# Performance work log

Hardware: AMD Instinct MI355X
Metric: run time of the kernel (lower is better)

The kernel has to match this reference:

```python
import jax, jax.numpy as jnp
import numpy as np
import math

B, CK, T, H, W = 4, 64, 8, 30, 54
N, CV = 8, 512

def setup_inputs() -> dict:
    key = jax.random.key(0)
    k1, k2, k3, k4 = jax.random.split(key, 4)
    mem_keys = jax.random.normal(k1, (B, CK, T, H, W), dtype=jnp.float32)
    mem_values = jax.random.normal(k2, (N, CV, T, H, W), dtype=jnp.float32)
    qk = jax.random.normal(k3, (B, CK, H, W), dtype=jnp.float32)
    broadcast_map = jax.random.randint(k4, (N,), 0, B, dtype=jnp.int64)
    return {"mem_keys": mem_keys, "mem_values": mem_values, "qk": qk,
            "broadcast_map": broadcast_map}

def reference(mem_keys, mem_values, qk, broadcast_map):
    # STCNModel.read_memory
    Bq, CKq, Tq, Hq, Wq = mem_keys.shape
    mk = mem_keys.reshape(Bq, CKq, Tq * Hq * Wq)      # [B, CK, THW]
    q = qk.reshape(Bq, CKq, Hq * Wq)                   # [B, CK, HW]
    a_sq = jnp.sum(mk * mk, axis=1)[:, :, None]        # [B, THW, 1]
    ab = jnp.einsum('bct,bcq->btq', mk, q)             # [B, THW, HW]
    frame_affinity = (2.0 * ab - a_sq) / math.sqrt(CKq)
    # softmax over memory dim (axis=1)
    frame_affinity = jax.nn.softmax(frame_affinity, axis=1)
    obj_affinity = frame_affinity[broadcast_map]       # [N, THW, HW]
    Nn, CVv = mem_values.shape[0], mem_values.shape[1]
    mo = mem_values.reshape(Nn, CVv, Tq * Hq * Wq)     # [N, CV, THW]
    obj_read = jnp.einsum('nct,ntq->ncq', mo, obj_affinity)
    return obj_read.reshape(Nn, CVv, Hq, Wq)
```

## Files before the change

kernel.cpp:

```cpp
#include <hip/hip_runtime.h>
#include <hip/hip_bf16.h>

#define CKDIM 64
#define THW   12960
#define HWDIM 1620
#define NOBJ  8
#define CVAL  512
#define NB    4
#define NSTEP 405
#define NJT   13
#define NCHS  8
#define NCHP  4
#define PCH   16
#define S2F   0.3606737602222409f

using bf16x8 = __attribute__((ext_vector_type(8))) short;
using f32x4  = __attribute__((ext_vector_type(4))) float;

__device__ __forceinline__ unsigned cvtpk(float lo, float hi) {
    unsigned r;
    asm("v_cvt_pk_bf16_f32 %0, %1, %2" : "=v"(r) : "v"(lo), "v"(hi));
    return r;
}
__device__ __forceinline__ unsigned short bf_rne(float x) {
    unsigned u = __float_as_uint(x);
    u += 0x7FFFu + ((u >> 16) & 1u);
    return (unsigned short)(u >> 16);
}
__device__ __forceinline__ float fexp2(float x) {
#if __has_builtin(__builtin_amdgcn_exp2f)
    return __builtin_amdgcn_exp2f(x);
#else
    return __expf(x * 0.69314718055994531f);
#endif
}

__global__ void stcn_ksq_kernel(const float* __restrict__ mk, float* __restrict__ k8l) {
    int t = blockIdx.x * 256 + threadIdx.x;
    if (t >= THW) return;
    int b = blockIdx.y;
    const float* p = mk + (size_t)b * CKDIM * THW + t;
    float s = 0.f;
#pragma unroll
    for (int c = 0; c < CKDIM; ++c) { float v = p[(size_t)c * THW]; s = fmaf(v, v, s); }
    k8l[b * THW + t] = s * (0.125f * 1.44269504088896341f);
}

__global__ __launch_bounds__(512)
void stcn_ktr_kernel(const float* __restrict__ mk, unsigned short* __restrict__ kbt) {
    __shared__ unsigned short L[64][72];
    const int tid = threadIdx.x, b = blockIdx.y, t0 = blockIdx.x * 64;
#pragma unroll
    for (int it = 0; it < 8; ++it) {
        int idx = tid + 512 * it;
        int tt = idx & 63, c = idx >> 6;
        int t = t0 + tt;
        float v = (t < THW) ? mk[((size_t)b * CKDIM + c) * THW + t] : 0.f;
        L[tt][c] = bf_rne(v);
    }
    __syncthreads();
    int tt = tid >> 3, cq = tid & 7;
    int t = t0 + tt;
    if (t < THW) {
        uint4 o = *(const uint4*)&L[tt][8 * cq];
        *(uint4*)(kbt + ((size_t)b * THW + t) * CKDIM + 8 * cq) = o;
    }
}

__global__ void stcn_vcvt_kernel(const float* __restrict__ mv, unsigned short* __restrict__ mvb) {
    size_t i = ((size_t)blockIdx.x * 256 + threadIdx.x) * 8;
    if (i >= (size_t)NOBJ * CVAL * THW) return;
    float4 v0 = *(const float4*)(mv + i);
    float4 v1 = *(const float4*)(mv + i + 4);
    uint4 o;
    o.x = cvtpk(v0.x, v0.y); o.y = cvtpk(v0.z, v0.w);
    o.z = cvtpk(v1.x, v1.y); o.w = cvtpk(v1.z, v1.w);
    *(uint4*)(mvb + i) = o;
}

template <int MODE, bool VB16, bool KB16>
__global__ __launch_bounds__(512, (MODE == 1) ? 4 : 1)
void stcn_aff_kernel(const float* __restrict__ mk, const unsigned short* __restrict__ kbt,
                     const float* __restrict__ qk, const float* __restrict__ k8l,
                     float* __restrict__ mpart, float* __restrict__ lpart,
                     const float* __restrict__ mv, const unsigned short* __restrict__ mvb,
                     const int* __restrict__ bmap, float* __restrict__ out)
{
    constexpr int SMEM_BYTES = (MODE == 0) ? 36864 : 45312;
    __shared__ __align__(16) unsigned char smem[SMEM_BYTES];
    unsigned short* KtP   = (unsigned short*)smem;
    float*          k8tP  = (float*)(smem + 9216);
    unsigned short* PtP   = (unsigned short*)(smem + 9472);
    unsigned short* VtP   = (unsigned short*)(smem + 23808);
    float*          mjsP  = (float*)(smem + 44288);
    float*          iljsP = (float*)(smem + 44800);
    unsigned short* QtP   = (unsigned short*)smem;

    const int tid  = threadIdx.x;
    const int w    = tid >> 6;
    const int lane = tid & 63;
    const int g    = lane >> 4;
    const int lr   = lane & 15;

    int b, n = 0, jt, kc, cb = 0;
    if (MODE == 0) { b = blockIdx.y; jt = blockIdx.x >> 3; kc = blockIdx.x & 7; }
    else {
        n = blockIdx.y; jt = blockIdx.x >> 3; kc = (blockIdx.x >> 1) & 3; cb = blockIdx.x & 1;
        b = bmap[n];
    }
    const int jbase = jt * 128;
    const int cbase = cb * 256;

#pragma unroll
    for (int it = 0; it < 8; ++it) {
        int idx = tid + 512 * it;
        int j = idx & 127, cp = idx >> 7;
        int jg = jbase + j;
        float q0 = 0.f, q1 = 0.f;
        if (jg < HWDIM) {
            const float* qp = qk + ((size_t)b * CKDIM + 2 * cp) * HWDIM + jg;
            q0 = qp[0]; q1 = qp[HWDIM];
        }
        unsigned wh = cvtpk(q0, q1);
        float r0 = q0 - __uint_as_float(wh << 16);
        float r1 = q1 - __uint_as_float(wh & 0xFFFF0000u);
        *(unsigned*)&QtP[(0 * 128 + j) * 72 + 2 * cp] = wh;
        *(unsigned*)&QtP[(1 * 128 + j) * 72 + 2 * cp] = cvtpk(r0, r1);
    }
    __syncthreads();
    bf16x8 bqh[2], bql[2];
#pragma unroll
    for (int s = 0; s < 2; ++s) {
        bqh[s] = *(const bf16x8*)&QtP[(0 * 128 + w * 16 + lr) * 72 + 32 * s + 8 * g];
        bql[s] = *(const bf16x8*)&QtP[(1 * 128 + w * 16 + lr) * 72 + 32 * s + 8 * g];
    }
    __syncthreads();

    auto stageK_loads = [&](int st, uint2& k16, float2* kvf) {
        if constexpr (KB16) {
            int tt = tid >> 4, cq = tid & 15;
            k16 = *(const uint2*)(kbt + ((size_t)b * THW + st * 32 + tt) * CKDIM + 4 * cq);
        } else {
#pragma unroll
            for (int it = 0; it < 2; ++it) {
                int idx = tid + 512 * it;
                int tt = idx & 31, cp = idx >> 5;
                const float* kp = mk + ((size_t)b * CKDIM + 2 * cp) * THW + st * 32 + tt;
                kvf[it].x = kp[0];
                kvf[it].y = kp[THW];
            }
        }
    };
    auto stageK_write = [&](int buf, uint2 k16, const float2* kvf) {
        if constexpr (KB16) {
            int tt = tid >> 4, cq = tid & 15;
            *(uint2*)&KtP[(buf * 32 + tt) * 72 + 4 * cq] = k16;
        } else {
#pragma unroll
            for (int it = 0; it < 2; ++it) {
                int idx = tid + 512 * it;
                int tt = idx & 31, cp = idx >> 5;
                *(unsigned*)&KtP[(buf * 32 + tt) * 72 + 2 * cp] = cvtpk(kvf[it].x, kvf[it].y);
            }
        }
    };

    int s0, s1;
    if (MODE == 0) { s0 = (NSTEP * kc) / NCHS; s1 = (NSTEP * (kc + 1)) / NCHS; }
    else           { s0 = (NSTEP * kc) / NCHP; s1 = (NSTEP * (kc + 1)) / NCHP; }

    if (MODE == 1 && tid < 128) {
        int jg = jbase + tid;
        float m = 0.f, l = 0.f;
        if (jg < HWDIM) {
            m = -1e30f;
#pragma unroll
            for (int c = 0; c < NCHS; ++c) {
                float mc = mpart[(b * NCHS + c) * HWDIM + jg];
                float lc = lpart[(b * NCHS + c) * HWDIM + jg];
                float mn = fmaxf(m, mc);
                l = l * fexp2(m - mn) + lc * fexp2(mc - mn);
                m = mn;
            }
        }
        mjsP[tid]  = m;
        iljsP[tid] = (l > 0.f) ? 1.f / l : 0.f;
    }
    {
        uint2 k16; float2 kvf[2];
        stageK_loads(s0, k16, kvf);
        stageK_write(0, k16, kvf);
        if (tid < 32) k8tP[tid] = k8l[b * THW + s0 * 32 + tid];
    }
    __syncthreads();

    float mv_j = 0.f, il_j = 0.f;
    if (MODE == 1) { mv_j = mjsP[w * 16 + lr]; il_j = iljsP[w * 16 + lr]; }

    float m_run = -1e30f, l_run = 0.f;
    f32x4 zz = {0.f, 0.f, 0.f, 0.f};
    f32x4 acc[4][4];
    if (MODE == 1)
#pragma unroll
        for (int i = 0; i < 4; ++i)
#pragma unroll
            for (int j = 0; j < 4; ++j) acc[i][j] = zz;

    const int wc = w >> 1, wj = w & 1;
    const int vc = tid >> 1, vth = tid & 1;

    int cur = 0;
    for (int st = s0; st < s1; ++st) {
        const int t0 = st * 32;
        const bool nxt = (st + 1 < s1);

        uint4 vw0 = {0,0,0,0}, vw1 = {0,0,0,0};
        if (MODE == 1) {
            if (VB16) {
                const unsigned short* vp = mvb + ((size_t)n * CVAL + cbase + vc) * THW + t0 + vth * 16;
                vw0 = *(const uint4*)vp;
                vw1 = *(const uint4*)(vp + 8);
            } else {
                const float* vp = mv + ((size_t)n * CVAL + cbase + vc) * THW + t0 + vth * 16;
                float4 f0 = *(const float4*)vp;
                float4 f1 = *(const float4*)(vp + 4);
                float4 f2 = *(const float4*)(vp + 8);
                float4 f3 = *(const float4*)(vp + 12);
                vw0 = make_uint4(cvtpk(f0.x,f0.y), cvtpk(f0.z,f0.w), cvtpk(f1.x,f1.y), cvtpk(f1.z,f1.w));
                vw1 = make_uint4(cvtpk(f2.x,f2.y), cvtpk(f2.z,f2.w), cvtpk(f3.x,f3.y), cvtpk(f3.z,f3.w));
            }
        }
        uint2 k16; float2 kvf[2];
        float k8next = 0.f;
        if (nxt) {
            stageK_loads(st + 1, k16, kvf);
            if (tid < 32) k8next = k8l[b * THW + (st + 1) * 32 + tid];
        }
        bf16x8 ak0[2], ak1[2];
#pragma unroll
        for (int s = 0; s < 2; ++s) {
            ak0[s] = *(const bf16x8*)&KtP[(cur * 32 + lr) * 72 + 32 * s + 8 * g];
            ak1[s] = *(const bf16x8*)&KtP[(cur * 32 + 16 + lr) * 72 + 32 * s + 8 * g];
        }
        f32x4 k80 = *(const f32x4*)&k8tP[cur * 32 + 4 * g];
        f32x4 k81 = *(const f32x4*)&k8tP[cur * 32 + 16 + 4 * g];
        f32x4 ab0 = zz, ab1 = zz;
#pragma unroll
        for (int s = 0; s < 2; ++s) {
            ab0 = __builtin_amdgcn_mfma_f32_16x16x32_bf16(ak0[s], bqh[s], ab0, 0, 0, 0);
            ab0 = __builtin_amdgcn_mfma_f32_16x16x32_bf16(ak0[s], bql[s], ab0, 0, 0, 0);
            ab1 = __builtin_amdgcn_mfma_f32_16x16x32_bf16(ak1[s], bqh[s], ab1, 0, 0, 0);
            ab1 = __builtin_amdgcn_mfma_f32_16x16x32_bf16(ak1[s], bql[s], ab1, 0, 0, 0);
        }
        if (nxt) {
            stageK_write(cur ^ 1, k16, kvf);
            if (tid < 32) k8tP[(cur ^ 1) * 32 + tid] = k8next;
        }

        if (MODE == 0) {
            float L0[4], L1[4], tmax = -1e30f;
#pragma unroll
            for (int r = 0; r < 4; ++r) {
                L0[r] = fmaf(ab0[r], S2F, -k80[r]); tmax = fmaxf(tmax, L0[r]);
                L1[r] = fmaf(ab1[r], S2F, -k81[r]); tmax = fmaxf(tmax, L1[r]);
            }
            float ps = 0.f;
#pragma unroll
            for (int r = 0; r < 4; ++r)
                ps += fexp2(L0[r] - tmax) + fexp2(L1[r] - tmax);
            float mn = fmaxf(m_run, tmax);
            l_run = l_run * fexp2(m_run - mn) + ps * fexp2(tmax - mn);
            m_run = mn;
            __syncthreads();
        } else {
            float p0[4], p1[4];
#pragma unroll
            for (int r = 0; r < 4; ++r) {
                p0[r] = fexp2(fmaf(ab0[r], S2F, -k80[r]) - mv_j) * il_j;
                p1[r] = fexp2(fmaf(ab1[r], S2F, -k81[r]) - mv_j) * il_j;
            }
            __syncthreads();
            {
                int jl = w * 16 + lr;
                *(uint2*)&PtP[jl * 56 + 4 * g]      = make_uint2(cvtpk(p0[0], p0[1]), cvtpk(p0[2], p0[3]));
                *(uint2*)&PtP[jl * 56 + 16 + 4 * g] = make_uint2(cvtpk(p1[0], p1[1]), cvtpk(p1[2], p1[3]));
                *(uint4*)&VtP[vc * 40 + vth * 16]     = vw0;
                *(uint4*)&VtP[vc * 40 + vth * 16 + 8] = vw1;
            }
            __syncthreads();
            bf16x8 bp[4];
#pragma unroll
            for (int jf = 0; jf < 4; ++jf)
                bp[jf] = *(const bf16x8*)&PtP[(wj * 64 + jf * 16 + lr) * 56 + 8 * g];
#pragma unroll
            for (int cf = 0; cf < 4; ++cf) {
                bf16x8 av = *(const bf16x8*)&VtP[(wc * 64 + cf * 16 + lr) * 40 + 8 * g];
#pragma unroll
                for (int jf = 0; jf < 4; ++jf)
                    acc[cf][jf] = __builtin_amdgcn_mfma_f32_16x16x32_bf16(av, bp[jf], acc[cf][jf], 0, 0, 0);
            }
        }
        cur ^= 1;
    }

    if (MODE == 0) {
#pragma unroll
        for (int off = 16; off < 64; off <<= 1) {
            float mo = __shfl_xor(m_run, off, 64);
            float lo = __shfl_xor(l_run, off, 64);
            float mn = fmaxf(m_run, mo);
            l_run = l_run * fexp2(m_run - mn) + lo * fexp2(mo - mn);
            m_run = mn;
        }
        int jg = jbase + w * 16 + lr;
        if (g == 0 && jg < HWDIM) {
            mpart[(b * NCHS + kc) * HWDIM + jg] = m_run;
            lpart[(b * NCHS + kc) * HWDIM + jg] = l_run;
        }
    } else {
#pragma unroll
        for (int cf = 0; cf < 4; ++cf) {
#pragma unroll
            for (int jf = 0; jf < 4; ++jf) {
                int jg = jbase + wj * 64 + jf * 16 + lr;
                if (jg < HWDIM) {
                    int c = cbase + wc * 64 + cf * 16 + 4 * g;
                    float* op = out + ((size_t)n * CVAL + c) * HWDIM + jg;
#pragma unroll
                    for (int r = 0; r < 4; ++r)
                        atomicAdd(op + (size_t)r * HWDIM, acc[cf][jf][r]);
                }
            }
        }
    }
}

__global__ __launch_bounds__(512)
void stcn_pwrite_kernel(const unsigned short* __restrict__ kbt,
                        const float* __restrict__ qk, const float* __restrict__ k8l,
                        const float* __restrict__ mpart, const float* __restrict__ lpart,
                        unsigned short* __restrict__ Pws, int phase)
{
    __shared__ __align__(16) unsigned char smem[36864];
    unsigned short* KtP   = (unsigned short*)smem;
    float*          k8tP  = (float*)(smem + 9216);
    unsigned short* PtP   = (unsigned short*)(smem + 9472);
    float*          mjsP  = (float*)(smem + 23808);
    float*          iljsP = (float*)(smem + 24320);
    unsigned short* QtP   = (unsigned short*)smem;

    const int tid  = threadIdx.x;
    const int w    = tid >> 6;
    const int lane = tid & 63;
    const int g    = lane >> 4;
    const int lr   = lane & 15;

    const int bb = blockIdx.y;
    const int b  = 2 * phase + bb;
    const int jt = blockIdx.x >> 4, kc = blockIdx.x & 15;
    const int jbase = jt * 128;

#pragma unroll
    for (int it = 0; it < 8; ++it) {
        int idx = tid + 512 * it;
        int j = idx & 127, cp = idx >> 7;
        int jg = jbase + j;
        float q0 = 0.f, q1 = 0.f;
        if (jg < HWDIM) {
            const float* qp = qk + ((size_t)b * CKDIM + 2 * cp) * HWDIM + jg;
            q0 = qp[0]; q1 = qp[HWDIM];
        }
        unsigned wh = cvtpk(q0, q1);
        float r0 = q0 - __uint_as_float(wh << 16);
        float r1 = q1 - __uint_as_float(wh & 0xFFFF0000u);
        *(unsigned*)&QtP[(0 * 128 + j) * 72 + 2 * cp] = wh;
        *(unsigned*)&QtP[(1 * 128 + j) * 72 + 2 * cp] = cvtpk(r0, r1);
    }
    __syncthreads();
    bf16x8 bqh[2], bql[2];
#pragma unroll
    for (int s = 0; s < 2; ++s) {
        bqh[s] = *(const bf16x8*)&QtP[(0 * 128 + w * 16 + lr) * 72 + 32 * s + 8 * g];
        bql[s] = *(const bf16x8*)&QtP[(1 * 128 + w * 16 + lr) * 72 + 32 * s + 8 * g];
    }
    __syncthreads();

    const int s0 = (NSTEP * kc) / PCH, s1 = (NSTEP * (kc + 1)) / PCH;

    if (tid < 128) {
        int jg = jbase + tid;
        float m = 0.f, l = 0.f;
        if (jg < HWDIM) {
            m = -1e30f;
#pragma unroll
            for (int c = 0; c < NCHS; ++c) {
                float mc = mpart[(b * NCHS + c) * HWDIM + jg];
                float lc = lpart[(b * NCHS + c) * HWDIM + jg];
                float mn = fmaxf(m, mc);
                l = l * fexp2(m - mn) + lc * fexp2(mc - mn);
                m = mn;
            }
        }
        mjsP[tid]  = m;
        iljsP[tid] = (l > 0.f) ? 1.f / l : 0.f;
    }
    {
        int tt = tid >> 4, cq = tid & 15;
        uint2 k16 = *(const uint2*)(kbt + ((size_t)b * THW + s0 * 32 + tt) * CKDIM + 4 * cq);
        *(uint2*)&KtP[tt * 72 + 4 * cq] = k16;
        if (tid < 32) k8tP[tid] = k8l[b * THW + s0 * 32 + tid];
    }
    __syncthreads();

    const float mv_j = mjsP[w * 16 + lr], il_j = iljsP[w * 16 + lr];
    f32x4 zz = {0.f, 0.f, 0.f, 0.f};

    int cur = 0;
    for (int st = s0; st < s1; ++st) {
        const int t0 = st * 32;
        const bool nxt = (st + 1 < s1);
        uint2 k16;
        float k8next = 0.f;
        const int tt = tid >> 4, cq = tid & 15;
        if (nxt) {
            k16 = *(const uint2*)(kbt + ((size_t)b * THW + (st + 1) * 32 + tt) * CKDIM + 4 * cq);
            if (tid < 32) k8next = k8l[b * THW + (st + 1) * 32 + tid];
        }
        bf16x8 ak0[2], ak1[2];
#pragma unroll
        for (int s = 0; s < 2; ++s) {
            ak0[s] = *(const bf16x8*)&KtP[(cur * 32 + lr) * 72 + 32 * s + 8 * g];
            ak1[s] = *(const bf16x8*)&KtP[(cur * 32 + 16 + lr) * 72 + 32 * s + 8 * g];
        }
        f32x4 k80 = *(const f32x4*)&k8tP[cur * 32 + 4 * g];
        f32x4 k81 = *(const f32x4*)&k8tP[cur * 32 + 16 + 4 * g];
        f32x4 ab0 = zz, ab1 = zz;
#pragma unroll
        for (int s = 0; s < 2; ++s) {
            ab0 = __builtin_amdgcn_mfma_f32_16x16x32_bf16(ak0[s], bqh[s], ab0, 0, 0, 0);
            ab0 = __builtin_amdgcn_mfma_f32_16x16x32_bf16(ak0[s], bql[s], ab0, 0, 0, 0);
            ab1 = __builtin_amdgcn_mfma_f32_16x16x32_bf16(ak1[s], bqh[s], ab1, 0, 0, 0);
            ab1 = __builtin_amdgcn_mfma_f32_16x16x32_bf16(ak1[s], bql[s], ab1, 0, 0, 0);
        }
        if (nxt) {
            *(uint2*)&KtP[((cur ^ 1) * 32 + tt) * 72 + 4 * cq] = k16;
            if (tid < 32) k8tP[(cur ^ 1) * 32 + tid] = k8next;
        }
        float p0[4], p1[4];
#pragma unroll
        for (int r = 0; r < 4; ++r) {
            p0[r] = fexp2(fmaf(ab0[r], S2F, -k80[r]) - mv_j) * il_j;
            p1[r] = fexp2(fmaf(ab1[r], S2F, -k81[r]) - mv_j) * il_j;
        }
        __syncthreads();
        {
            int jl = w * 16 + lr;
            *(uint2*)&PtP[jl * 56 + 4 * g]      = make_uint2(cvtpk(p0[0], p0[1]), cvtpk(p0[2], p0[3]));
            *(uint2*)&PtP[jl * 56 + 16 + 4 * g] = make_uint2(cvtpk(p1[0], p1[1]), cvtpk(p1[2], p1[3]));
        }
        __syncthreads();
        {
            int jr = tid >> 2, qq = tid & 3;
            int jg = jbase + jr;
            if (jg < HWDIM)
                *(uint4*)(Pws + ((size_t)bb * HWDIM + jg) * THW + t0 + qq * 8) =
                    *(const uint4*)&PtP[jr * 56 + qq * 8];
        }
        cur ^= 1;
    }
}

__global__ __launch_bounds__(512, 4)
void stcn_gemm_kernel(const unsigned short* __restrict__ mvb,
                      const unsigned short* __restrict__ Pws,
                      const int* __restrict__ bmap, float* __restrict__ out, int phase)
{
    __shared__ __align__(16) unsigned short Av[2][128 * 40];
    __shared__ __align__(16) unsigned short Bv[2][128 * 40];

    const int n = blockIdx.y;
    const int b = bmap[n];
    if ((b >> 1) != phase) return;
    const int bb = b & 1;
    const int x  = blockIdx.x;
    const int ks = x & 1;
    const int jn = (x >> 1) % NJT;
    const int cm = (x >> 1) / NJT;
    const int jbase = jn * 128, cb2 = cm * 128;

    const int tid = threadIdx.x, w = tid >> 6, lane = tid & 63, g = lane >> 4, lr = lane & 15;
    const int wc = w >> 2, wjj = w & 3;
    const int row = tid >> 2, q = tid & 3;

    const unsigned short* vsrc = mvb + ((size_t)n * CVAL + cb2 + row) * THW + q * 8;
    const int jrow = jbase + row;
    const bool jok = jrow < HWDIM;
    const unsigned short* psrc = Pws + ((size_t)bb * HWDIM + (jok ? jrow : 0)) * THW + q * 8;

    const int s0 = (NSTEP * ks) / 2, s1 = (NSTEP * (ks + 1)) / 2;

    f32x4 zz = {0.f, 0.f, 0.f, 0.f};
    f32x4 acc[4][2];
#pragma unroll
    for (int i = 0; i < 4; ++i) { acc[i][0] = zz; acc[i][1] = zz; }

    {
        uint4 a = *(const uint4*)(vsrc + s0 * 32);
        uint4 p = jok ? *(const uint4*)(psrc + s0 * 32) : make_uint4(0, 0, 0, 0);
        *(uint4*)&Av[0][row * 40 + q * 8] = a;
        *(uint4*)&Bv[0][row * 40 + q * 8] = p;
    }
    __syncthreads();

    int cur = 0;
    for (int st = s0; st < s1; ++st) {
        const bool nxt = (st + 1 < s1);
        uint4 a, p;
        if (nxt) {
            a = *(const uint4*)(vsrc + (size_t)(st + 1) * 32);
            p = jok ? *(const uint4*)(psrc + (size_t)(st + 1) * 32) : make_uint4(0, 0, 0, 0);
        }
        bf16x8 av[4], bp[2];
#pragma unroll
        for (int cf = 0; cf < 4; ++cf)
            av[cf] = *(const bf16x8*)&Av[cur][(wc * 64 + cf * 16 + lr) * 40 + 8 * g];
#pragma unroll
        for (int jf = 0; jf < 2; ++jf)
            bp[jf] = *(const bf16x8*)&Bv[cur][(wjj * 32 + jf * 16 + lr) * 40 + 8 * g];
#pragma unroll
        for (int cf = 0; cf < 4; ++cf)
#pragma unroll
            for (int jf = 0; jf < 2; ++jf)
                acc[cf][jf] = __builtin_amdgcn_mfma_f32_16x16x32_bf16(av[cf], bp[jf], acc[cf][jf], 0, 0, 0);
        if (nxt) {
            *(uint4*)&Av[cur ^ 1][row * 40 + q * 8] = a;
            *(uint4*)&Bv[cur ^ 1][row * 40 + q * 8] = p;
        }
        __syncthreads();
        cur ^= 1;
    }

#pragma unroll
    for (int cf = 0; cf < 4; ++cf)
#pragma unroll
        for (int jf = 0; jf < 2; ++jf) {
            int jg = jbase + wjj * 32 + jf * 16 + lr;
            if (jg < HWDIM) {
                int c = cb2 + wc * 64 + cf * 16 + 4 * g;
                float* op = out + ((size_t)n * CVAL + c) * HWDIM + jg;
#pragma unroll
                for (int r = 0; r < 4; ++r)
                    atomicAdd(op + (size_t)r * HWDIM, acc[cf][jf][r]);
            }
        }
}

extern "C" void kernel_launch(void* const* d_in, const int* in_sizes, int n_in,
                              void* d_out, int out_size, void* d_ws, size_t ws_size,
                              hipStream_t stream) {
    (void)in_sizes; (void)n_in;
    const float* mk   = (const float*)d_in[0];
    const float* mv   = (const float*)d_in[1];
    const float* qkp  = (const float*)d_in[2];
    const int*   bmap = (const int*)d_in[3];
    float* out = (float*)d_out;

    float* k8l   = (float*)d_ws;
    float* mpart = k8l + NB * THW;
    float* lpart = mpart + NB * NCHS * HWDIM;
    unsigned short* mvb = (unsigned short*)(lpart + NB * NCHS * HWDIM);
    unsigned short* kbt = mvb + (size_t)NOBJ * CVAL * THW;
    unsigned short* Pws = kbt + (size_t)NB * THW * CKDIM;

    size_t base_bytes = (size_t)(NB * THW + 2 * NB * NCHS * HWDIM) * 4;
    size_t need_vb  = base_bytes + (size_t)NOBJ * CVAL * THW * 2;
    size_t need_kbt = need_vb + (size_t)NB * THW * CKDIM * 2;
    size_t need_P   = need_kbt + (size_t)2 * HWDIM * THW * 2;
    bool use_vb16 = (ws_size >= need_vb);
    bool use_kbt  = (ws_size >= need_kbt);
    bool use_P    = (ws_size >= need_P);

    hipMemsetAsync(d_out, 0, (size_t)out_size * sizeof(float), stream);
    stcn_ksq_kernel<<<dim3((THW + 255) / 256, NB), 256, 0, stream>>>(mk, k8l);
    if (use_kbt)
        stcn_ktr_kernel<<<dim3((THW + 63) / 64, NB), 512, 0, stream>>>(mk, kbt);
    if (use_vb16) {
        size_t nthreads = (size_t)NOBJ * CVAL * THW / 8;
        stcn_vcvt_kernel<<<(unsigned)((nthreads + 255) / 256), 256, 0, stream>>>(mv, mvb);
    }

    if (use_kbt)
        stcn_aff_kernel<0, false, true><<<dim3(NJT * NCHS, NB), 512, 0, stream>>>(
            mk, kbt, qkp, k8l, mpart, lpart, nullptr, nullptr, nullptr, nullptr);
    else
        stcn_aff_kernel<0, false, false><<<dim3(NJT * NCHS, NB), 512, 0, stream>>>(
            mk, nullptr, qkp, k8l, mpart, lpart, nullptr, nullptr, nullptr, nullptr);

    if (use_P) {
        for (int p = 0; p < 2; ++p) {
            stcn_pwrite_kernel<<<dim3(NJT * PCH, 2), 512, 0, stream>>>(
                kbt, qkp, k8l, mpart, lpart, Pws, p);
            stcn_gemm_kernel<<<dim3(2 * NJT * 4, NOBJ), 512, 0, stream>>>(
                mvb, Pws, bmap, out, p);
        }
    } else {
        dim3 g1(NJT * NCHP * 2, NOBJ);
        if (use_vb16 && use_kbt)
            stcn_aff_kernel<1, true, true><<<g1, 512, 0, stream>>>(
                mk, kbt, qkp, k8l, mpart, lpart, nullptr, mvb, bmap, out);
        else if (use_vb16)
            stcn_aff_kernel<1, true, false><<<g1, 512, 0, stream>>>(
                mk, nullptr, qkp, k8l, mpart, lpart, nullptr, mvb, bmap, out);
        else
            stcn_aff_kernel<1, false, false><<<g1, 512, 0, stream>>>(
                mk, nullptr, qkp, k8l, mpart, lpart, mv, nullptr, bmap, out);
    }
}
```

Baseline: 571.2 us.

## Use 256x128 GEMM tiles with 4-way split-K, two-stage prefetch, single-phase P

Replaces the value-by-probability GEMM with a version that uses 256-channel by 128-position tiles and 4x4 MFMA fragments per wave. The K dimension is split four ways instead of two, and global loads are register-prefetched two steps ahead. When the workspace is large enough, probabilities for all four batches are written in one pass so a single GEMM launch covers every object, instead of two alternating phases. The larger tiles raise register and LDS pressure, and the extra split-K ways add more atomic adds on the output.

```diff
diff --git a/kernel.cpp b/kernel.cpp
--- a/kernel.cpp
+++ b/kernel.cpp
@@ -339,7 +339,7 @@
 void stcn_pwrite_kernel(const unsigned short* __restrict__ kbt,
                         const float* __restrict__ qk, const float* __restrict__ k8l,
                         const float* __restrict__ mpart, const float* __restrict__ lpart,
-                        unsigned short* __restrict__ Pws, int phase)
+                        unsigned short* __restrict__ Pws, int bbase)
 {
     __shared__ __align__(16) unsigned char smem[36864];
     unsigned short* KtP   = (unsigned short*)smem;
@@ -356,7 +356,7 @@
     const int lr   = lane & 15;
 
     const int bb = blockIdx.y;
-    const int b  = 2 * phase + bb;
+    const int b  = bbase + bb;
     const int jt = blockIdx.x >> 4, kc = blockIdx.x & 15;
     const int jbase = jt * 128;
 
@@ -470,83 +470,98 @@
     }
 }
 
+template <bool FULLP>
 __global__ __launch_bounds__(512, 4)
-void stcn_gemm_kernel(const unsigned short* __restrict__ mvb,
-                      const unsigned short* __restrict__ Pws,
-                      const int* __restrict__ bmap, float* __restrict__ out, int phase)
+void stcn_gemm2_kernel(const unsigned short* __restrict__ mvb,
+                       const unsigned short* __restrict__ Pws,
+                       const int* __restrict__ bmap, float* __restrict__ out, int phase)
 {
-    __shared__ __align__(16) unsigned short Av[2][128 * 40];
+    __shared__ __align__(16) unsigned short Av[2][256 * 40];
     __shared__ __align__(16) unsigned short Bv[2][128 * 40];
 
     const int n = blockIdx.y;
     const int b = bmap[n];
-    if ((b >> 1) != phase) return;
-    const int bb = b & 1;
-    const int x  = blockIdx.x;
-    const int ks = x & 1;
-    const int jn = (x >> 1) % NJT;
-    const int cm = (x >> 1) / NJT;
-    const int jbase = jn * 128, cb2 = cm * 128;
+    int bslot;
+    if constexpr (FULLP) { bslot = b; }
+    else { if ((b >> 1) != phase) return; bslot = b & 1; }
+
+    const int x    = blockIdx.x;
+    const int ks   = x & 3;
+    const int rest = x >> 2;
+    const int jn   = rest % NJT;
+    const int cm   = rest / NJT;
+    const int jbase = jn * 128, cbase = cm * 256;
 
     const int tid = threadIdx.x, w = tid >> 6, lane = tid & 63, g = lane >> 4, lr = lane & 15;
-    const int wc = w >> 2, wjj = w & 3;
-    const int row = tid >> 2, q = tid & 3;
-
-    const unsigned short* vsrc = mvb + ((size_t)n * CVAL + cb2 + row) * THW + q * 8;
-    const int jrow = jbase + row;
+    const int wc = w >> 1, wj = w & 1;
+
+    const int arow = tid >> 1, at = (tid & 1) * 16;
+    const int brow = tid >> 2, bt = (tid & 3) * 8;
+    const unsigned short* vsrc = mvb + ((size_t)n * CVAL + cbase + arow) * THW + at;
+    const int jrow = jbase + brow;
     const bool jok = jrow < HWDIM;
-    const unsigned short* psrc = Pws + ((size_t)bb * HWDIM + (jok ? jrow : 0)) * THW + q * 8;
-
-    const int s0 = (NSTEP * ks) / 2, s1 = (NSTEP * (ks + 1)) / 2;
+    const unsigned short* psrc = Pws + ((size_t)bslot * HWDIM + (jok ? jrow : 0)) * THW + bt;
+
+    const int s0 = (NSTEP * ks) / 4, s1 = (NSTEP * (ks + 1)) / 4;
 
     f32x4 zz = {0.f, 0.f, 0.f, 0.f};
-    f32x4 acc[4][2];
-#pragma unroll
-    for (int i = 0; i < 4; ++i) { acc[i][0] = zz; acc[i][1] = zz; }
-
+    f32x4 acc[4][4];
+#pragma unroll
+    for (int i = 0; i < 4; ++i)
+#pragma unroll
+        for (int j = 0; j < 4; ++j) acc[i][j] = zz;
+
+    const uint4 zq = make_uint4(0, 0, 0, 0);
     {
-        uint4 a = *(const uint4*)(vsrc + s0 * 32);
-        uint4 p = jok ? *(const uint4*)(psrc + s0 * 32) : make_uint4(0, 0, 0, 0);
-        *(uint4*)&Av[0][row * 40 + q * 8] = a;
-        *(uint4*)&Bv[0][row * 40 + q * 8] = p;
-    }
+        uint4 ta0 = *(const uint4*)(vsrc + (size_t)s0 * 32);
+        uint4 ta1 = *(const uint4*)(vsrc + (size_t)s0 * 32 + 8);
+        uint4 tb0 = jok ? *(const uint4*)(psrc + (size_t)s0 * 32) : zq;
+        *(uint4*)&Av[0][arow * 40 + at]     = ta0;
+        *(uint4*)&Av[0][arow * 40 + at + 8] = ta1;
+        *(uint4*)&Bv[0][brow * 40 + bt]     = tb0;
+    }
+    uint4 nA0 = *(const uint4*)(vsrc + (size_t)(s0 + 1) * 32);
+    uint4 nA1 = *(const uint4*)(vsrc + (size_t)(s0 + 1) * 32 + 8);
+    uint4 nB0 = jok ? *(const uint4*)(psrc + (size_t)(s0 + 1) * 32) : zq;
     __syncthreads();
 
     int cur = 0;
     for (int st = s0; st < s1; ++st) {
-        const bool nxt = (st + 1 < s1);
-        uint4 a, p;
-        if (nxt) {
-            a = *(const uint4*)(vsrc + (size_t)(st + 1) * 32);
-            p = jok ? *(const uint4*)(psrc + (size_t)(st + 1) * 32) : make_uint4(0, 0, 0, 0);
-        }
-        bf16x8 av[4], bp[2];
-#pragma unroll
-        for (int cf = 0; cf < 4; ++cf)
-            av[cf] = *(const bf16x8*)&Av[cur][(wc * 64 + cf * 16 + lr) * 40 + 8 * g];
-#pragma unroll
-        for (int jf = 0; jf < 2; ++jf)
-            bp[jf] = *(const bf16x8*)&Bv[cur][(wjj * 32 + jf * 16 + lr) * 40 + 8 * g];
-#pragma unroll
-        for (int cf = 0; cf < 4; ++cf)
-#pragma unroll
-            for (int jf = 0; jf < 2; ++jf)
-                acc[cf][jf] = __builtin_amdgcn_mfma_f32_16x16x32_bf16(av[cf], bp[jf], acc[cf][jf], 0, 0, 0);
-        if (nxt) {
-            *(uint4*)&Av[cur ^ 1][row * 40 + q * 8] = a;
-            *(uint4*)&Bv[cur ^ 1][row * 40 + q * 8] = p;
+        const bool h1 = (st + 1 < s1), h2 = (st + 2 < s1);
+        uint4 fA0, fA1, fB0;
+        if (h2) {
+            fA0 = *(const uint4*)(vsrc + (size_t)(st + 2) * 32);
+            fA1 = *(const uint4*)(vsrc + (size_t)(st + 2) * 32 + 8);
+            fB0 = jok ? *(const uint4*)(psrc + (size_t)(st + 2) * 32) : zq;
+        }
+        bf16x8 bp[4];
+#pragma unroll
+        for (int jf = 0; jf < 4; ++jf)
+            bp[jf] = *(const bf16x8*)&Bv[cur][(wj * 64 + jf * 16 + lr) * 40 + 8 * g];
+        if (h1) {
+            *(uint4*)&Av[cur ^ 1][arow * 40 + at]     = nA0;
+            *(uint4*)&Av[cur ^ 1][arow * 40 + at + 8] = nA1;
+            *(uint4*)&Bv[cur ^ 1][brow * 40 + bt]     = nB0;
+        }
+#pragma unroll
+        for (int cf = 0; cf < 4; ++cf) {
+            bf16x8 av = *(const bf16x8*)&Av[cur][(wc * 64 + cf * 16 + lr) * 40 + 8 * g];
+#pragma unroll
+            for (int jf = 0; jf < 4; ++jf)
+                acc[cf][jf] = __builtin_amdgcn_mfma_f32_16x16x32_bf16(av, bp[jf], acc[cf][jf], 0, 0, 0);
         }
         __syncthreads();
+        if (h2) { nA0 = fA0; nA1 = fA1; nB0 = fB0; }
         cur ^= 1;
     }
 
 #pragma unroll
     for (int cf = 0; cf < 4; ++cf)
 #pragma unroll
-        for (int jf = 0; jf < 2; ++jf) {
-            int jg = jbase + wjj * 32 + jf * 16 + lr;
+        for (int jf = 0; jf < 4; ++jf) {
+            int jg = jbase + wj * 64 + jf * 16 + lr;
             if (jg < HWDIM) {
-                int c = cb2 + wc * 64 + cf * 16 + 4 * g;
+                int c = cbase + wc * 64 + cf * 16 + 4 * g;
                 float* op = out + ((size_t)n * CVAL + c) * HWDIM + jg;
 #pragma unroll
                 for (int r = 0; r < 4; ++r)
@@ -575,10 +590,12 @@
     size_t base_bytes = (size_t)(NB * THW + 2 * NB * NCHS * HWDIM) * 4;
     size_t need_vb  = base_bytes + (size_t)NOBJ * CVAL * THW * 2;
     size_t need_kbt = need_vb + (size_t)NB * THW * CKDIM * 2;
-    size_t need_P   = need_kbt + (size_t)2 * HWDIM * THW * 2;
+    size_t need_P2  = need_kbt + (size_t)2 * HWDIM * THW * 2;
+    size_t need_P4  = need_kbt + (size_t)4 * HWDIM * THW * 2;
     bool use_vb16 = (ws_size >= need_vb);
     bool use_kbt  = (ws_size >= need_kbt);
-    bool use_P    = (ws_size >= need_P);
+    bool use_P2   = (ws_size >= need_P2);
+    bool use_P4   = (ws_size >= need_P4);
 
     hipMemsetAsync(d_out, 0, (size_t)out_size * sizeof(float), stream);
     stcn_ksq_kernel<<<dim3((THW + 255) / 256, NB), 256, 0, stream>>>(mk, k8l);
@@ -596,11 +613,16 @@
         stcn_aff_kernel<0, false, false><<<dim3(NJT * NCHS, NB), 512, 0, stream>>>(
             mk, nullptr, qkp, k8l, mpart, lpart, nullptr, nullptr, nullptr, nullptr);
 
-    if (use_P) {
+    if (use_P4 && use_kbt) {
+        stcn_pwrite_kernel<<<dim3(NJT * PCH, NB), 512, 0, stream>>>(
+            kbt, qkp, k8l, mpart, lpart, Pws, 0);
+        stcn_gemm2_kernel<true><<<dim3(104, NOBJ), 512, 0, stream>>>(
+            mvb, Pws, bmap, out, 0);
+    } else if (use_P2 && use_kbt) {
         for (int p = 0; p < 2; ++p) {
             stcn_pwrite_kernel<<<dim3(NJT * PCH, 2), 512, 0, stream>>>(
-                kbt, qkp, k8l, mpart, lpart, Pws, p);
-            stcn_gemm_kernel<<<dim3(2 * NJT * 4, NOBJ), 512, 0, stream>>>(
+                kbt, qkp, k8l, mpart, lpart, Pws, 2 * p);
+            stcn_gemm2_kernel<false><<<dim3(104, NOBJ), 512, 0, stream>>>(
                 mvb, Pws, bmap, out, p);
         }
     } else {
```

Result: faster. 554.1 us (-3.0%).
